# Performance work log

Hardware: AMD Instinct MI355X
Metric: run time of the kernel (lower is better)

The kernel has to match this reference:

```python
import jax, jax.numpy as jnp
import numpy as np

N_NODES = 100000
N_EDGES = 1600000
N_GRAPHS = 512
DIM = 64


def gcn_conv(x, W, b, src, dst, n):
    # PyG GCNConv: h = x @ W; add self-loops; symmetric norm D^-1/2 (A+I) D^-1/2; aggregate; + bias
    h = x @ W  # [N, H]
    loop = jnp.arange(n, dtype=src.dtype)
    s = jnp.concatenate([src, loop])
    d = jnp.concatenate([dst, loop])
    deg = jax.ops.segment_sum(jnp.ones_like(d, dtype=h.dtype), d, num_segments=n)  # in-degree incl self-loop
    dinv = jnp.where(deg > 0, jax.lax.rsqrt(deg), 0.0)
    norm = dinv[s] * dinv[d]  # [E+N]
    msg = h[s] * norm[:, None]  # gather + scale
    out = jax.ops.segment_sum(msg, d, num_segments=n)  # scatter-add
    return out + b


def global_mean_pool(x, batch, num_graphs):
    sums = jax.ops.segment_sum(x, batch, num_segments=num_graphs)
    cnts = jax.ops.segment_sum(jnp.ones((x.shape[0],), x.dtype), batch, num_segments=num_graphs)
    return sums / jnp.maximum(cnts, 1.0)[:, None]


def setup_inputs() -> dict:
    key = jax.random.key(0)
    ks = jax.random.split(key, 12)
    scale = 1.0 / np.sqrt(DIM)
    x = jax.random.normal(ks[0], (N_NODES, DIM), jnp.float32)
    edge_index = jax.random.randint(ks[1], (2, N_EDGES), 0, N_NODES, dtype=jnp.int64)
    batch = jnp.sort(jax.random.randint(ks[2], (N_NODES,), 0, N_GRAPHS, dtype=jnp.int64))
    W1 = jax.random.normal(ks[3], (DIM, DIM), jnp.float32) * scale
    b1 = jnp.zeros((DIM,), jnp.float32)
    W2 = jax.random.normal(ks[4], (DIM, DIM), jnp.float32) * scale
    b2 = jnp.zeros((DIM,), jnp.float32)
    W3 = jax.random.normal(ks[5], (DIM, DIM), jnp.float32) * scale
    b3 = jnp.zeros((DIM,), jnp.float32)
    W4 = jax.random.normal(ks[6], (DIM, 1), jnp.float32) * scale
    b4 = jnp.zeros((1,), jnp.float32)
    return {"x": x, "edge_index": edge_index, "batch": batch,
            "W1": W1, "b1": b1, "W2": W2, "b2": b2,
            "W3": W3, "b3": b3, "W4": W4, "b4": b4}


def reference(x, edge_index, batch, W1, b1, W2, b2, W3, b3, W4, b4):
    src, dst = edge_index[0], edge_index[1]
    h = gcn_conv(x, W1, b1, src, dst, N_NODES)
    h = jax.nn.relu(h)
    h = gcn_conv(h, W2, b2, src, dst, N_NODES)
    g = global_mean_pool(h, batch, N_GRAPHS)  # [G, H]
    g = jax.nn.relu(g @ W3 + b3)
    pred = (g @ W4 + b4).reshape(-1)  # [G]
    return pred
```

## Files before the change

### kernel.cpp

```cpp
#include <hip/hip_runtime.h>
#include <math.h>


#define NBLK 3125

__global__ __launch_bounds__(256) void k_init(float* gsum, int* blockCnt,
                                              int gsz, int nblk) {
  int i = blockIdx.x * 256 + threadIdx.x;
  if (i < gsz) gsum[i] = 0.f;
  if (i < nblk + 64) blockCnt[i] = 0;
}

__global__ __launch_bounds__(256) void k_histB(const int* __restrict__ dst,
                                               int* __restrict__ blockCnt,
                                               int e, int nblk) {
  __shared__ int h[3200];
  int t = threadIdx.x;
  for (int i = t; i < 3200; i += 256) h[i] = 0;
  __syncthreads();
  int base = blockIdx.x * 8192;
#pragma unroll
  for (int k = 0; k < 32; ++k) {
    int i = base + k * 256 + t;
    if (i < e) atomicAdd(&h[dst[i] >> 5], 1);
  }
  __syncthreads();
  for (int i = t; i < nblk; i += 256) {
    int v = h[i];
    if (v) atomicAdd(&blockCnt[i], v);
  }
}

__global__ __launch_bounds__(256) void k_scan(const int* __restrict__ blockCnt,
                                              int* __restrict__ blockBase,
                                              int* __restrict__ blockCursor,
                                              int* __restrict__ bucketCursor,
                                              int nblk, int nbuck) {
  __shared__ int wsum[4];
  int t = threadIdx.x;
  int w = t >> 6, lane = t & 63;
  int ch = (nblk + 255) >> 8;
  int lo = t * ch;
  int hi = lo + ch;
  if (hi > nblk) hi = nblk;
  int s = 0;
  for (int i = lo; i < hi; ++i) s += blockCnt[i];
  int inc = s;
  for (int off = 1; off < 64; off <<= 1) {
    int u = __shfl_up(inc, off);
    if (lane >= off) inc += u;
  }
  if (lane == 63) wsum[w] = inc;
  __syncthreads();
  int wpre = 0;
  for (int i = 0; i < w; ++i) wpre += wsum[i];
  int run = wpre + inc - s;
  for (int i = lo; i < hi; ++i) {
    int v = blockCnt[i];
    blockBase[i] = run;
    blockCursor[i] = run;
    if ((i & 63) == 0 && (i >> 6) < nbuck) bucketCursor[i >> 6] = run;
    run += v;
  }
  if (t == 0) blockBase[nblk] = wsum[0] + wsum[1] + wsum[2] + wsum[3];
}

__global__ __launch_bounds__(256) void k_p1(const int* __restrict__ src,
                                            const int* __restrict__ dst,
                                            int* __restrict__ bucketCursor,
                                            int* __restrict__ tmp, int e) {
  __shared__ int hist[64];
  __shared__ int gbase[64];
  int t = threadIdx.x;
  int base = blockIdx.x * 2048;
  if (t < 64) hist[t] = 0;
  __syncthreads();
  int ent[8], rk[8], bk[8];
#pragma unroll
  for (int k = 0; k < 8; ++k) {
    int i = base + k * 256 + t;
    bool v = i < e;
    int s = v ? src[i] : 0;
    int d = v ? dst[i] : 0;
    bk[k] = d >> 11;
    ent[k] = (((d >> 5) & 63) << 22) | (s << 5) | (d & 31);
    rk[k] = v ? atomicAdd(&hist[bk[k]], 1) : -1;
  }
  __syncthreads();
  if (t < 64 && hist[t] > 0) gbase[t] = atomicAdd(&bucketCursor[t], hist[t]);
  __syncthreads();
#pragma unroll
  for (int k = 0; k < 8; ++k)
    if (rk[k] >= 0) tmp[gbase[bk[k]] + rk[k]] = ent[k];
}

__global__ __launch_bounds__(256) void k_p2(const int* __restrict__ blockBase,
                                            const int* __restrict__ tmp,
                                            int* __restrict__ blockCursor,
                                            int* __restrict__ csr, int nblk) {
  __shared__ int hist[64];
  __shared__ int gbase[64];
  int b = blockIdx.x >> 3;
  int sl = blockIdx.x & 7;
  int hiIdx = (b + 1) << 6;
  if (hiIdx > nblk) hiIdx = nblk;
  int lo_b = blockBase[b << 6];
  int hi_b = blockBase[hiIdx];
  int len = hi_b - lo_b;
  int lo = lo_b + (int)(((long long)len * sl) >> 3);
  int hi = lo_b + (int)(((long long)len * (sl + 1)) >> 3);
  int t = threadIdx.x;
  for (int rbase = lo; rbase < hi; rbase += 2048) {
    if (t < 64) hist[t] = 0;
    __syncthreads();
    int ent[8], rk[8], bin[8];
#pragma unroll
    for (int k = 0; k < 8; ++k) {
      int i = rbase + k * 256 + t;
      bool v = i < hi;
      int en = v ? tmp[i] : 0;
      ent[k] = en;
      bin[k] = en >> 22;
      rk[k] = v ? atomicAdd(&hist[bin[k]], 1) : -1;
    }
    __syncthreads();
    if (t < 64 && hist[t] > 0)
      gbase[t] = atomicAdd(&blockCursor[(b << 6) + t], hist[t]);
    __syncthreads();
#pragma unroll
    for (int k = 0; k < 8; ++k)
      if (rk[k] >= 0) csr[gbase[bin[k]] + rk[k]] = ent[k] & 0x3FFFFF;
    __syncthreads();
  }
}

__global__ __launch_bounds__(256) void k_bsort(const int* __restrict__ blockBase,
                                               int* __restrict__ csr,
                                               float* __restrict__ dinv,
                                               int* __restrict__ segLo,
                                               int* __restrict__ segHi, int n) {
  __shared__ int in_sh[1024];
  __shared__ int out_sh[1024];
  __shared__ int hist[128];
  __shared__ int hscan[129];
  __shared__ int deg[32];
  int blk = blockIdx.x;
  int nodeBase = blk << 5;
  if (nodeBase >= n) return;
  int p0 = blockBase[blk];
  int p1 = blockBase[blk + 1];
  int seg = p1 - p0;
  int t = threadIdx.x;
  if (t < 32) deg[t] = 0;
  if (t == 0) {
    segLo[2 * blk] = p0;
    segHi[2 * blk] = p1;
    segLo[2 * blk + 1] = p0;
    segHi[2 * blk + 1] = p1;
  }
  __syncthreads();
  for (int i = t; i < seg; i += 256) atomicAdd(&deg[csr[p0 + i] & 31], 1);
  __syncthreads();
  if (t < 32 && nodeBase + t < n)
    dinv[nodeBase + t] = 1.0f / sqrtf((float)(deg[t] + 1));
  if (seg <= 0 || seg > 1024) return;
  if (t < 128) hist[t] = 0;
  __syncthreads();
  for (int i = t; i < seg; i += 256) {
    int v = csr[p0 + i];
    in_sh[i] = v;
    atomicAdd(&hist[((v & 16) << 2) | ((v >> 16) & 63)], 1);
  }
  __syncthreads();
  if (t == 0) {
    int s = 0;
    for (int b = 0; b < 128; ++b) {
      hscan[b] = s;
      s += hist[b];
    }
    hscan[128] = s;
  }
  __syncthreads();
  int cntLow = hscan[64];
  __syncthreads();
  for (int i = t; i < seg; i += 256) {
    int v = in_sh[i];
    int pos = atomicAdd(&hscan[((v & 16) << 2) | ((v >> 16) & 63)], 1);
    out_sh[pos] = v;
  }
  __syncthreads();
  for (int i = t; i < seg; i += 256) csr[p0 + i] = out_sh[i];
  if (t == 0) {
    segHi[2 * blk] = p0 + cntLow;
    segLo[2 * blk + 1] = p0 + cntLow;
  }
}

__global__ __launch_bounds__(256) void k_gemm64s(const float* __restrict__ X,
                                                 const float* __restrict__ W,
                                                 const float* __restrict__ dinv,
                                                 float* __restrict__ Y, int n) {
  __shared__ float Xs[64 * 65];
  __shared__ float Ws[64 * 64];
  int t = threadIdx.x;
  int r0 = blockIdx.x << 6;
  for (int i = t * 4; i < 4096; i += 1024)
    *(float4*)&Ws[i] = *(const float4*)&W[i];
  for (int s = t; s < 1024; s += 256) {
    int r = s >> 4, c4 = (s & 15) << 2;
    float4 v = make_float4(0.f, 0.f, 0.f, 0.f);
    if (r0 + r < n) v = *(const float4*)&X[(size_t)(r0 + r) * 64 + c4];
    Xs[r * 65 + c4 + 0] = v.x;
    Xs[r * 65 + c4 + 1] = v.y;
    Xs[r * 65 + c4 + 2] = v.z;
    Xs[r * 65 + c4 + 3] = v.w;
  }
  __syncthreads();
  int c4 = (t & 15) << 2;
  int rb = (t >> 4) << 2;
  float4 a0 = {0, 0, 0, 0}, a1 = {0, 0, 0, 0}, a2 = {0, 0, 0, 0}, a3 = {0, 0, 0, 0};
  for (int k = 0; k < 64; ++k) {
    float4 w = *(const float4*)&Ws[k * 64 + c4];
    float x0 = Xs[(rb + 0) * 65 + k];
    float x1 = Xs[(rb + 1) * 65 + k];
    float x2 = Xs[(rb + 2) * 65 + k];
    float x3 = Xs[(rb + 3) * 65 + k];
    a0.x += x0 * w.x; a0.y += x0 * w.y; a0.z += x0 * w.z; a0.w += x0 * w.w;
    a1.x += x1 * w.x; a1.y += x1 * w.y; a1.z += x1 * w.z; a1.w += x1 * w.w;
    a2.x += x2 * w.x; a2.y += x2 * w.y; a2.z += x2 * w.z; a2.w += x2 * w.w;
    a3.x += x3 * w.x; a3.y += x3 * w.y; a3.z += x3 * w.z; a3.w += x3 * w.w;
  }
  int r = r0 + rb;
  if (r + 0 < n) {
    float s0 = dinv[r + 0];
    a0.x *= s0; a0.y *= s0; a0.z *= s0; a0.w *= s0;
    *(float4*)&Y[(size_t)(r + 0) * 64 + c4] = a0;
  }
  if (r + 1 < n) {
    float s1 = dinv[r + 1];
    a1.x *= s1; a1.y *= s1; a1.z *= s1; a1.w *= s1;
    *(float4*)&Y[(size_t)(r + 1) * 64 + c4] = a1;
  }
  if (r + 2 < n) {
    float s2 = dinv[r + 2];
    a2.x *= s2; a2.y *= s2; a2.z *= s2; a2.w *= s2;
    *(float4*)&Y[(size_t)(r + 2) * 64 + c4] = a2;
  }
  if (r + 3 < n) {
    float s3 = dinv[r + 3];
    a3.x *= s3; a3.y *= s3; a3.z *= s3; a3.w *= s3;
    *(float4*)&Y[(size_t)(r + 3) * 64 + c4] = a3;
  }
}

template <int POOL>
__global__ __launch_bounds__(256) void k_agg(
    const float* __restrict__ Hs, const int* __restrict__ csr,
    const int* __restrict__ segLo, const int* __restrict__ segHi,
    const float* __restrict__ dinv, const float* __restrict__ bias,
    const int* __restrict__ batch, float* __restrict__ outv,
    float* __restrict__ gsum, int n, int ntask) {
  __shared__ float accs[4][16 * 64];
  int t = threadIdx.x;
  int w = t >> 6, lane = t & 63;
  int task = blockIdx.x * 4 + w;
  if (task >= ntask) return;
  int nodeBase = task << 4;
  int par = task & 1;
  float* a = accs[w];
#pragma unroll 4
  for (int d = 0; d < 16; ++d) a[d * 64 + lane] = 0.f;
  int p0 = segLo[task];
  int p1 = segHi[task];
  int c = p1 - p0;
  if (c > 0) {
    int sub = lane & 31;
    int qlast = p1 - 1;
    int qq = p0 + sub;
    int pk = csr[qq < qlast ? qq : qlast];
    for (int rb = 0; rb < c; rb += 32) {
      int pk_next = 0;
      bool more = (rb + 32) < c;
      if (more) {
        int qn = p0 + rb + 32 + sub;
        pk_next = csr[qn < qlast ? qn : qlast];
      }
      int rem = c - rb;
      int ee[32];
#pragma unroll
      for (int k = 0; k < 32; ++k) ee[k] = __builtin_amdgcn_readlane(pk, k);
      float tv[32];
#pragma unroll
      for (int k = 0; k < 32; ++k)
        tv[k] = Hs[(size_t)(ee[k] >> 5) * 64 + lane];
#pragma unroll
      for (int k = 0; k < 32; ++k)
        if (k < rem && (((ee[k] >> 4) & 1) == par))
          a[(ee[k] & 15) * 64 + lane] += tv[k];
      pk = pk_next;
    }
  }
  for (int d = 0; d < 16; ++d) {
    int node = nodeBase + d;
    if (node >= n) break;
    float dn = dinv[node];
    float v = a[d * 64 + lane] + Hs[(size_t)node * 64 + lane];
    v = v * dn + bias[lane];
    if (POOL) {
      int g = batch[node];
      atomicAdd(&gsum[(size_t)g * 64 + lane], v);
    } else {
      outv[(size_t)node * 64 + lane] = fmaxf(v, 0.f);
    }
  }
}

__global__ __launch_bounds__(256) void k_head(
    const float* __restrict__ gsum, const int* __restrict__ batch,
    const float* __restrict__ W3, const float* __restrict__ b3,
    const float* __restrict__ W4, const float* __restrict__ b4,
    float* __restrict__ out, int ng, int n) {
  int wid = (blockIdx.x * 256 + threadIdx.x) >> 6;
  int lane = threadIdx.x & 63;
  if (wid >= ng) return;
  int lo = 0, hi = n;
  while (lo < hi) {
    int mid = (lo + hi) >> 1;
    if (batch[mid] < wid) lo = mid + 1; else hi = mid;
  }
  int lb = lo;
  hi = n;
  while (lo < hi) {
    int mid = (lo + hi) >> 1;
    if (batch[mid] <= wid) lo = mid + 1; else hi = mid;
  }
  float cden = fmaxf((float)(lo - lb), 1.0f);
  float m = gsum[(size_t)wid * 64 + lane] / cden;
  float acc = b3[lane];
  for (int k = 0; k < 64; ++k) {
    float mk = __shfl(m, k);
    acc += mk * W3[k * 64 + lane];
  }
  acc = fmaxf(acc, 0.f);
  float r = acc * W4[lane];
  for (int off = 32; off; off >>= 1) r += __shfl_down(r, off);
  if (lane == 0) out[wid] = r + b4[0];
}

extern "C" void kernel_launch(void* const* d_in, const int* in_sizes, int n_in,
                              void* d_out, int out_size, void* d_ws, size_t ws_size,
                              hipStream_t stream) {
  const float* x = (const float*)d_in[0];
  const int* edge = (const int*)d_in[1];
  const int* batch = (const int*)d_in[2];
  const float* W1 = (const float*)d_in[3];
  const float* b1 = (const float*)d_in[4];
  const float* W2 = (const float*)d_in[5];
  const float* b2 = (const float*)d_in[6];
  const float* W3 = (const float*)d_in[7];
  const float* b3 = (const float*)d_in[8];
  const float* W4 = (const float*)d_in[9];
  const float* b4 = (const float*)d_in[10];
  float* out = (float*)d_out;

  const int n = in_sizes[0] / 64;
  const int e = in_sizes[1] / 2;
  const int ng = out_size;
  const int* src = edge;
  const int* dst = edge + e;

  char* ws = (char*)d_ws;
  size_t off = 0;
  auto alloc = [&](size_t bytes) -> void* {
    void* p = ws + off;
    off = (off + bytes + 255) & ~(size_t)255;
    return p;
  };
  float* A = (float*)alloc((size_t)n * 64 * 4);
  float* B = (float*)alloc((size_t)n * 64 * 4);
  float* dinv = (float*)alloc((size_t)n * 4);
  int* blockCnt = (int*)alloc(3264 * 4);
  int* blockBase = (int*)alloc(3264 * 4);
  int* blockCursor = (int*)alloc(3264 * 4);
  int* bucketCursor = (int*)alloc(64 * 4);
  int* segLo = (int*)alloc(6400 * 4);
  int* segHi = (int*)alloc(6400 * 4);
  int* csr = (int*)alloc((size_t)e * 4);
  float* gsum = (float*)alloc((size_t)ng * 64 * 4);
  int* tmp = (int*)B;

  const int nblk = (n + 31) / 32;
  const int nbuck = (nblk + 63) / 64;
  const int ntask = 2 * nblk;
  const int nagg = (ntask + 3) / 4;
  const int gsz = ng * 64;

  int zmax = gsz > nblk + 64 ? gsz : nblk + 64;
  k_init<<<(zmax + 255) / 256, 256, 0, stream>>>(gsum, blockCnt, gsz, nblk);
  k_histB<<<(e + 8191) / 8192, 256, 0, stream>>>(dst, blockCnt, e, nblk);
  k_scan<<<1, 256, 0, stream>>>(blockCnt, blockBase, blockCursor, bucketCursor,
                                nblk, nbuck);
  k_p1<<<(e + 2047) / 2048, 256, 0, stream>>>(src, dst, bucketCursor, tmp, e);
  k_p2<<<nbuck * 8, 256, 0, stream>>>(blockBase, tmp, blockCursor, csr, nblk);
  k_bsort<<<nblk, 256, 0, stream>>>(blockBase, csr, dinv, segLo, segHi, n);

  k_gemm64s<<<(n + 63) / 64, 256, 0, stream>>>(x, W1, dinv, A, n);
  k_agg<0><<<nagg, 256, 0, stream>>>(A, csr, segLo, segHi, dinv, b1, batch, B,
                                     gsum, n, ntask);
  k_gemm64s<<<(n + 63) / 64, 256, 0, stream>>>(B, W2, dinv, A, n);
  k_agg<1><<<nagg, 256, 0, stream>>>(A, csr, segLo, segHi, dinv, b2, batch, B,
                                     gsum, n, ntask);
  k_head<<<((size_t)ng * 64 + 255) / 256, 256, 0, stream>>>(gsum, batch, W3, b3,
                                                            W4, b4, out, ng, n);
}
```

Measured before the change: 323.3 us.

## Reorder GCN as aggregate-then-transform, move second GEMM into pooled head, split tasks by four

Uses linearity to aggregate raw features before multiplying by W1. This drops one full-graph GEMM, since the second layer's W2 and bias are applied after mean pooling in the head kernel. The aggregation now applies the source dinv per edge, which adds an extra gather per edge. Work is partitioned into four sub-tasks of 8 nodes per 32-node block instead of two of 16, giving more waves with smaller shared accumulators at the cost of re-scanning each edge segment four times.

New measurement: 344.4 us. 6.5% more time.

```diff
diff --git a/kernel.cpp b/kernel.cpp
--- a/kernel.cpp
+++ b/kernel.cpp
@@ -141,8 +141,8 @@
                                                int* __restrict__ segHi, int n) {
   __shared__ int in_sh[1024];
   __shared__ int out_sh[1024];
-  __shared__ int hist[128];
-  __shared__ int hscan[129];
+  __shared__ int hist[256];
+  __shared__ int hscan[256];
   __shared__ int deg[32];
   int blk = blockIdx.x;
   int nodeBase = blk << 5;
@@ -152,11 +152,9 @@
   int seg = p1 - p0;
   int t = threadIdx.x;
   if (t < 32) deg[t] = 0;
-  if (t == 0) {
-    segLo[2 * blk] = p0;
-    segHi[2 * blk] = p1;
-    segLo[2 * blk + 1] = p0;
-    segHi[2 * blk + 1] = p1;
+  if (t < 4) {
+    segLo[4 * blk + t] = p0;
+    segHi[4 * blk + t] = p1;
   }
   __syncthreads();
   for (int i = t; i < seg; i += 256) atomicAdd(&deg[csr[p0 + i] & 31], 1);
@@ -164,42 +162,47 @@
   if (t < 32 && nodeBase + t < n)
     dinv[nodeBase + t] = 1.0f / sqrtf((float)(deg[t] + 1));
   if (seg <= 0 || seg > 1024) return;
-  if (t < 128) hist[t] = 0;
+  hist[t] = 0;
   __syncthreads();
   for (int i = t; i < seg; i += 256) {
     int v = csr[p0 + i];
     in_sh[i] = v;
-    atomicAdd(&hist[((v & 16) << 2) | ((v >> 16) & 63)], 1);
+    atomicAdd(&hist[(((v >> 3) & 3) << 6) | ((v >> 16) & 63)], 1);
   }
   __syncthreads();
   if (t == 0) {
     int s = 0;
-    for (int b = 0; b < 128; ++b) {
+    for (int b = 0; b < 256; ++b) {
       hscan[b] = s;
       s += hist[b];
     }
-    hscan[128] = s;
-  }
-  __syncthreads();
-  int cntLow = hscan[64];
+  }
+  __syncthreads();
+  int q1 = hscan[64];
+  int q2 = hscan[128];
+  int q3 = hscan[192];
   __syncthreads();
   for (int i = t; i < seg; i += 256) {
     int v = in_sh[i];
-    int pos = atomicAdd(&hscan[((v & 16) << 2) | ((v >> 16) & 63)], 1);
+    int pos = atomicAdd(&hscan[(((v >> 3) & 3) << 6) | ((v >> 16) & 63)], 1);
     out_sh[pos] = v;
   }
   __syncthreads();
   for (int i = t; i < seg; i += 256) csr[p0 + i] = out_sh[i];
   if (t == 0) {
-    segHi[2 * blk] = p0 + cntLow;
-    segLo[2 * blk + 1] = p0 + cntLow;
-  }
-}
-
-__global__ __launch_bounds__(256) void k_gemm64s(const float* __restrict__ X,
-                                                 const float* __restrict__ W,
-                                                 const float* __restrict__ dinv,
-                                                 float* __restrict__ Y, int n) {
+    segHi[4 * blk + 0] = p0 + q1;
+    segLo[4 * blk + 1] = p0 + q1;
+    segHi[4 * blk + 1] = p0 + q2;
+    segLo[4 * blk + 2] = p0 + q2;
+    segHi[4 * blk + 2] = p0 + q3;
+    segLo[4 * blk + 3] = p0 + q3;
+  }
+}
+
+__global__ __launch_bounds__(256) void k_gemm64br(const float* __restrict__ X,
+                                                  const float* __restrict__ W,
+                                                  const float* __restrict__ bias,
+                                                  float* __restrict__ Y, int n) {
   __shared__ float Xs[64 * 65];
   __shared__ float Ws[64 * 64];
   int t = threadIdx.x;
@@ -230,46 +233,46 @@
     a2.x += x2 * w.x; a2.y += x2 * w.y; a2.z += x2 * w.z; a2.w += x2 * w.w;
     a3.x += x3 * w.x; a3.y += x3 * w.y; a3.z += x3 * w.z; a3.w += x3 * w.w;
   }
+  float4 bb = *(const float4*)&bias[c4];
   int r = r0 + rb;
   if (r + 0 < n) {
-    float s0 = dinv[r + 0];
-    a0.x *= s0; a0.y *= s0; a0.z *= s0; a0.w *= s0;
+    a0.x = fmaxf(a0.x + bb.x, 0.f); a0.y = fmaxf(a0.y + bb.y, 0.f);
+    a0.z = fmaxf(a0.z + bb.z, 0.f); a0.w = fmaxf(a0.w + bb.w, 0.f);
     *(float4*)&Y[(size_t)(r + 0) * 64 + c4] = a0;
   }
   if (r + 1 < n) {
-    float s1 = dinv[r + 1];
-    a1.x *= s1; a1.y *= s1; a1.z *= s1; a1.w *= s1;
+    a1.x = fmaxf(a1.x + bb.x, 0.f); a1.y = fmaxf(a1.y + bb.y, 0.f);
+    a1.z = fmaxf(a1.z + bb.z, 0.f); a1.w = fmaxf(a1.w + bb.w, 0.f);
     *(float4*)&Y[(size_t)(r + 1) * 64 + c4] = a1;
   }
   if (r + 2 < n) {
-    float s2 = dinv[r + 2];
-    a2.x *= s2; a2.y *= s2; a2.z *= s2; a2.w *= s2;
+    a2.x = fmaxf(a2.x + bb.x, 0.f); a2.y = fmaxf(a2.y + bb.y, 0.f);
+    a2.z = fmaxf(a2.z + bb.z, 0.f); a2.w = fmaxf(a2.w + bb.w, 0.f);
     *(float4*)&Y[(size_t)(r + 2) * 64 + c4] = a2;
   }
   if (r + 3 < n) {
-    float s3 = dinv[r + 3];
-    a3.x *= s3; a3.y *= s3; a3.z *= s3; a3.w *= s3;
+    a3.x = fmaxf(a3.x + bb.x, 0.f); a3.y = fmaxf(a3.y + bb.y, 0.f);
+    a3.z = fmaxf(a3.z + bb.z, 0.f); a3.w = fmaxf(a3.w + bb.w, 0.f);
     *(float4*)&Y[(size_t)(r + 3) * 64 + c4] = a3;
   }
 }
 
 template <int POOL>
 __global__ __launch_bounds__(256) void k_agg(
-    const float* __restrict__ Hs, const int* __restrict__ csr,
+    const float* __restrict__ X, const int* __restrict__ csr,
     const int* __restrict__ segLo, const int* __restrict__ segHi,
-    const float* __restrict__ dinv, const float* __restrict__ bias,
-    const int* __restrict__ batch, float* __restrict__ outv,
-    float* __restrict__ gsum, int n, int ntask) {
-  __shared__ float accs[4][16 * 64];
+    const float* __restrict__ dinv, const int* __restrict__ batch,
+    float* __restrict__ outv, float* __restrict__ gsum, int n, int ntask) {
+  __shared__ float accs[4][8 * 64];
   int t = threadIdx.x;
   int w = t >> 6, lane = t & 63;
   int task = blockIdx.x * 4 + w;
   if (task >= ntask) return;
-  int nodeBase = task << 4;
-  int par = task & 1;
+  int nodeBase = task << 3;
+  int par = task & 3;
   float* a = accs[w];
-#pragma unroll 4
-  for (int d = 0; d < 16; ++d) a[d * 64 + lane] = 0.f;
+#pragma unroll
+  for (int d = 0; d < 8; ++d) a[d * 64 + lane] = 0.f;
   int p0 = segLo[task];
   int p1 = segHi[task];
   int c = p1 - p0;
@@ -289,34 +292,37 @@
       int ee[32];
 #pragma unroll
       for (int k = 0; k < 32; ++k) ee[k] = __builtin_amdgcn_readlane(pk, k);
-      float tv[32];
+      float tv[32], dv[32];
+#pragma unroll
+      for (int k = 0; k < 32; ++k) {
+        int sr = ee[k] >> 5;
+        tv[k] = X[(size_t)sr * 64 + lane];
+        dv[k] = dinv[sr];
+      }
 #pragma unroll
       for (int k = 0; k < 32; ++k)
-        tv[k] = Hs[(size_t)(ee[k] >> 5) * 64 + lane];
-#pragma unroll
-      for (int k = 0; k < 32; ++k)
-        if (k < rem && (((ee[k] >> 4) & 1) == par))
-          a[(ee[k] & 15) * 64 + lane] += tv[k];
+        if (k < rem && (((ee[k] >> 3) & 3) == par))
+          a[(ee[k] & 7) * 64 + lane] += tv[k] * dv[k];
       pk = pk_next;
     }
   }
-  for (int d = 0; d < 16; ++d) {
+  for (int d = 0; d < 8; ++d) {
     int node = nodeBase + d;
     if (node >= n) break;
     float dn = dinv[node];
-    float v = a[d * 64 + lane] + Hs[(size_t)node * 64 + lane];
-    v = v * dn + bias[lane];
+    float v = (a[d * 64 + lane] + X[(size_t)node * 64 + lane] * dn) * dn;
     if (POOL) {
       int g = batch[node];
       atomicAdd(&gsum[(size_t)g * 64 + lane], v);
     } else {
-      outv[(size_t)node * 64 + lane] = fmaxf(v, 0.f);
+      outv[(size_t)node * 64 + lane] = v;
     }
   }
 }
 
 __global__ __launch_bounds__(256) void k_head(
     const float* __restrict__ gsum, const int* __restrict__ batch,
+    const float* __restrict__ W2, const float* __restrict__ b2,
     const float* __restrict__ W3, const float* __restrict__ b3,
     const float* __restrict__ W4, const float* __restrict__ b4,
     float* __restrict__ out, int ng, int n) {
@@ -336,13 +342,18 @@
   }
   float cden = fmaxf((float)(lo - lb), 1.0f);
   float m = gsum[(size_t)wid * 64 + lane] / cden;
-  float acc = b3[lane];
+  float g2 = b2[lane];
   for (int k = 0; k < 64; ++k) {
     float mk = __shfl(m, k);
-    acc += mk * W3[k * 64 + lane];
-  }
-  acc = fmaxf(acc, 0.f);
-  float r = acc * W4[lane];
+    g2 += mk * W2[k * 64 + lane];
+  }
+  float g3 = b3[lane];
+  for (int k = 0; k < 64; ++k) {
+    float gk = __shfl(g2, k);
+    g3 += gk * W3[k * 64 + lane];
+  }
+  g3 = fmaxf(g3, 0.f);
+  float r = g3 * W4[lane];
   for (int off = 32; off; off >>= 1) r += __shfl_down(r, off);
   if (lane == 0) out[wid] = r + b4[0];
 }
@@ -383,15 +394,15 @@
   int* blockBase = (int*)alloc(3264 * 4);
   int* blockCursor = (int*)alloc(3264 * 4);
   int* bucketCursor = (int*)alloc(64 * 4);
-  int* segLo = (int*)alloc(6400 * 4);
-  int* segHi = (int*)alloc(6400 * 4);
+  int* segLo = (int*)alloc(12544 * 4);
+  int* segHi = (int*)alloc(12544 * 4);
   int* csr = (int*)alloc((size_t)e * 4);
   float* gsum = (float*)alloc((size_t)ng * 64 * 4);
   int* tmp = (int*)B;
 
   const int nblk = (n + 31) / 32;
   const int nbuck = (nblk + 63) / 64;
-  const int ntask = 2 * nblk;
+  const int ntask = 4 * nblk;
   const int nagg = (ntask + 3) / 4;
   const int gsz = ng * 64;
 
@@ -404,12 +415,11 @@
   k_p2<<<nbuck * 8, 256, 0, stream>>>(blockBase, tmp, blockCursor, csr, nblk);
   k_bsort<<<nblk, 256, 0, stream>>>(blockBase, csr, dinv, segLo, segHi, n);
 
-  k_gemm64s<<<(n + 63) / 64, 256, 0, stream>>>(x, W1, dinv, A, n);
-  k_agg<0><<<nagg, 256, 0, stream>>>(A, csr, segLo, segHi, dinv, b1, batch, B,
+  k_agg<0><<<nagg, 256, 0, stream>>>(x, csr, segLo, segHi, dinv, batch, B,
                                      gsum, n, ntask);
-  k_gemm64s<<<(n + 63) / 64, 256, 0, stream>>>(B, W2, dinv, A, n);
-  k_agg<1><<<nagg, 256, 0, stream>>>(A, csr, segLo, segHi, dinv, b2, batch, B,
+  k_gemm64br<<<(n + 63) / 64, 256, 0, stream>>>(B, W1, b1, A, n);
+  k_agg<1><<<nagg, 256, 0, stream>>>(A, csr, segLo, segHi, dinv, batch, B,
                                      gsum, n, ntask);
-  k_head<<<((size_t)ng * 64 + 255) / 256, 256, 0, stream>>>(gsum, batch, W3, b3,
-                                                            W4, b4, out, ng, n);
-}
+  k_head<<<((size_t)ng * 64 + 255) / 256, 256, 0, stream>>>(
+      gsum, batch, W2, b2, W3, b3, W4, b4, out, ng, n);
+}
```

## Reorder GCN aggregation before matmul and fold second layer weights into pooled head

Applied to the files above, without the earlier changes.

Uses linearity to aggregate first and multiply by weights afterwards. Layer 1 now prescales x by dinv and aggregates, then a GEMM applies W1, bias, ReLU and the dinv prescale for layer 2. Layer 2 aggregates without a GEMM, and W2 plus b2 are applied after mean pooling in the head, which removes one full node-level GEMM pass. The aggregation block size is also halved to 128 threads, trading fewer waves per block for more blocks. Rounding order changes slightly.

After: 319.8 us. About the same (-1.1%).

```diff
diff --git a/kernel.cpp b/kernel.cpp
--- a/kernel.cpp
+++ b/kernel.cpp
@@ -196,10 +196,23 @@
   }
 }
 
-__global__ __launch_bounds__(256) void k_gemm64s(const float* __restrict__ X,
-                                                 const float* __restrict__ W,
-                                                 const float* __restrict__ dinv,
-                                                 float* __restrict__ Y, int n) {
+__global__ __launch_bounds__(256) void k_prescale(const float* __restrict__ x,
+                                                  const float* __restrict__ dinv,
+                                                  float* __restrict__ P, int n) {
+  int i = blockIdx.x * 256 + threadIdx.x;
+  int total = n * 16;
+  if (i >= total) return;
+  float4 v = *(const float4*)&x[(size_t)i * 4];
+  float s = dinv[i >> 4];
+  v.x *= s; v.y *= s; v.z *= s; v.w *= s;
+  *(float4*)&P[(size_t)i * 4] = v;
+}
+
+__global__ __launch_bounds__(256) void k_gemm64brs(const float* __restrict__ X,
+                                                   const float* __restrict__ W,
+                                                   const float* __restrict__ bias,
+                                                   const float* __restrict__ dinv,
+                                                   float* __restrict__ Y, int n) {
   __shared__ float Xs[64 * 65];
   __shared__ float Ws[64 * 64];
   int t = threadIdx.x;
@@ -230,40 +243,44 @@
     a2.x += x2 * w.x; a2.y += x2 * w.y; a2.z += x2 * w.z; a2.w += x2 * w.w;
     a3.x += x3 * w.x; a3.y += x3 * w.y; a3.z += x3 * w.z; a3.w += x3 * w.w;
   }
+  float4 bb = *(const float4*)&bias[c4];
   int r = r0 + rb;
   if (r + 0 < n) {
     float s0 = dinv[r + 0];
-    a0.x *= s0; a0.y *= s0; a0.z *= s0; a0.w *= s0;
+    a0.x = fmaxf(a0.x + bb.x, 0.f) * s0; a0.y = fmaxf(a0.y + bb.y, 0.f) * s0;
+    a0.z = fmaxf(a0.z + bb.z, 0.f) * s0; a0.w = fmaxf(a0.w + bb.w, 0.f) * s0;
     *(float4*)&Y[(size_t)(r + 0) * 64 + c4] = a0;
   }
   if (r + 1 < n) {
     float s1 = dinv[r + 1];
-    a1.x *= s1; a1.y *= s1; a1.z *= s1; a1.w *= s1;
+    a1.x = fmaxf(a1.x + bb.x, 0.f) * s1; a1.y = fmaxf(a1.y + bb.y, 0.f) * s1;
+    a1.z = fmaxf(a1.z + bb.z, 0.f) * s1; a1.w = fmaxf(a1.w + bb.w, 0.f) * s1;
     *(float4*)&Y[(size_t)(r + 1) * 64 + c4] = a1;
   }
   if (r + 2 < n) {
     float s2 = dinv[r + 2];
-    a2.x *= s2; a2.y *= s2; a2.z *= s2; a2.w *= s2;
+    a2.x = fmaxf(a2.x + bb.x, 0.f) * s2; a2.y = fmaxf(a2.y + bb.y, 0.f) * s2;
+    a2.z = fmaxf(a2.z + bb.z, 0.f) * s2; a2.w = fmaxf(a2.w + bb.w, 0.f) * s2;
     *(float4*)&Y[(size_t)(r + 2) * 64 + c4] = a2;
   }
   if (r + 3 < n) {
     float s3 = dinv[r + 3];
-    a3.x *= s3; a3.y *= s3; a3.z *= s3; a3.w *= s3;
+    a3.x = fmaxf(a3.x + bb.x, 0.f) * s3; a3.y = fmaxf(a3.y + bb.y, 0.f) * s3;
+    a3.z = fmaxf(a3.z + bb.z, 0.f) * s3; a3.w = fmaxf(a3.w + bb.w, 0.f) * s3;
     *(float4*)&Y[(size_t)(r + 3) * 64 + c4] = a3;
   }
 }
 
 template <int POOL>
-__global__ __launch_bounds__(256) void k_agg(
-    const float* __restrict__ Hs, const int* __restrict__ csr,
+__global__ __launch_bounds__(128) void k_agg(
+    const float* __restrict__ X, const int* __restrict__ csr,
     const int* __restrict__ segLo, const int* __restrict__ segHi,
-    const float* __restrict__ dinv, const float* __restrict__ bias,
-    const int* __restrict__ batch, float* __restrict__ outv,
-    float* __restrict__ gsum, int n, int ntask) {
-  __shared__ float accs[4][16 * 64];
+    const float* __restrict__ dinv, const int* __restrict__ batch,
+    float* __restrict__ outv, float* __restrict__ gsum, int n, int ntask) {
+  __shared__ float accs[2][16 * 64];
   int t = threadIdx.x;
   int w = t >> 6, lane = t & 63;
-  int task = blockIdx.x * 4 + w;
+  int task = blockIdx.x * 2 + w;
   if (task >= ntask) return;
   int nodeBase = task << 4;
   int par = task & 1;
@@ -292,7 +309,7 @@
       float tv[32];
 #pragma unroll
       for (int k = 0; k < 32; ++k)
-        tv[k] = Hs[(size_t)(ee[k] >> 5) * 64 + lane];
+        tv[k] = X[(size_t)(ee[k] >> 5) * 64 + lane];
 #pragma unroll
       for (int k = 0; k < 32; ++k)
         if (k < rem && (((ee[k] >> 4) & 1) == par))
@@ -304,19 +321,19 @@
     int node = nodeBase + d;
     if (node >= n) break;
     float dn = dinv[node];
-    float v = a[d * 64 + lane] + Hs[(size_t)node * 64 + lane];
-    v = v * dn + bias[lane];
+    float v = (a[d * 64 + lane] + X[(size_t)node * 64 + lane]) * dn;
     if (POOL) {
       int g = batch[node];
       atomicAdd(&gsum[(size_t)g * 64 + lane], v);
     } else {
-      outv[(size_t)node * 64 + lane] = fmaxf(v, 0.f);
+      outv[(size_t)node * 64 + lane] = v;
     }
   }
 }
 
 __global__ __launch_bounds__(256) void k_head(
     const float* __restrict__ gsum, const int* __restrict__ batch,
+    const float* __restrict__ W2, const float* __restrict__ b2,
     const float* __restrict__ W3, const float* __restrict__ b3,
     const float* __restrict__ W4, const float* __restrict__ b4,
     float* __restrict__ out, int ng, int n) {
@@ -336,13 +353,18 @@
   }
   float cden = fmaxf((float)(lo - lb), 1.0f);
   float m = gsum[(size_t)wid * 64 + lane] / cden;
-  float acc = b3[lane];
+  float g2 = b2[lane];
   for (int k = 0; k < 64; ++k) {
     float mk = __shfl(m, k);
-    acc += mk * W3[k * 64 + lane];
-  }
-  acc = fmaxf(acc, 0.f);
-  float r = acc * W4[lane];
+    g2 += mk * W2[k * 64 + lane];
+  }
+  float g3 = b3[lane];
+  for (int k = 0; k < 64; ++k) {
+    float gk = __shfl(g2, k);
+    g3 += gk * W3[k * 64 + lane];
+  }
+  g3 = fmaxf(g3, 0.f);
+  float r = g3 * W4[lane];
   for (int off = 32; off; off >>= 1) r += __shfl_down(r, off);
   if (lane == 0) out[wid] = r + b4[0];
 }
@@ -392,7 +414,7 @@
   const int nblk = (n + 31) / 32;
   const int nbuck = (nblk + 63) / 64;
   const int ntask = 2 * nblk;
-  const int nagg = (ntask + 3) / 4;
+  const int nagg = (ntask + 1) / 2;
   const int gsz = ng * 64;
 
   int zmax = gsz > nblk + 64 ? gsz : nblk + 64;
@@ -404,12 +426,12 @@
   k_p2<<<nbuck * 8, 256, 0, stream>>>(blockBase, tmp, blockCursor, csr, nblk);
   k_bsort<<<nblk, 256, 0, stream>>>(blockBase, csr, dinv, segLo, segHi, n);
 
-  k_gemm64s<<<(n + 63) / 64, 256, 0, stream>>>(x, W1, dinv, A, n);
-  k_agg<0><<<nagg, 256, 0, stream>>>(A, csr, segLo, segHi, dinv, b1, batch, B,
+  k_prescale<<<(n * 16 + 255) / 256, 256, 0, stream>>>(x, dinv, A, n);
+  k_agg<0><<<nagg, 128, 0, stream>>>(A, csr, segLo, segHi, dinv, batch, B,
                                      gsum, n, ntask);
-  k_gemm64s<<<(n + 63) / 64, 256, 0, stream>>>(B, W2, dinv, A, n);
-  k_agg<1><<<nagg, 256, 0, stream>>>(A, csr, segLo, segHi, dinv, b2, batch, B,
+  k_gemm64brs<<<(n + 63) / 64, 256, 0, stream>>>(B, W1, b1, dinv, A, n);
+  k_agg<1><<<nagg, 128, 0, stream>>>(A, csr, segLo, segHi, dinv, batch, B,
                                      gsum, n, ntask);
-  k_head<<<((size_t)ng * 64 + 255) / 256, 256, 0, stream>>>(gsum, batch, W3, b3,
-                                                            W4, b4, out, ng, n);
-}
+  k_head<<<((size_t)ng * 64 + 255) / 256, 256, 0, stream>>>(
+      gsum, batch, W2, b2, W3, b3, W4, b4, out, ng, n);
+}
```
